# Optimization experiments

Hardware: AMD Instinct MI355X
Metric: run time of the kernel (lower is better)

## Reference

```python
import jax, jax.numpy as jnp
import numpy as np

D_MODEL = 512
NUM_HEADS = 8
D_FF = 2048
HEAD_DIM = D_MODEL // NUM_HEADS
EPS = 1e-8


def rmsnorm(x, scale):
    rms = jax.lax.rsqrt(jnp.mean(x * x, axis=-1, keepdims=True) + EPS)
    return scale * x * rms


def alibi_bias(seq_len, num_heads):
    # faithful to: 1.0 / (arange(1,H+1) * 2**arange(0,8)[:,None]).flatten()[:H]
    a = jnp.arange(1, num_heads + 1, dtype=jnp.float32)          # (H,)
    b = 2.0 ** jnp.arange(0, 8, dtype=jnp.float32)[:, None]       # (8,1)
    slopes = (1.0 / (a * b).reshape(-1))[:num_heads]               # (H,)
    pos = jnp.arange(seq_len)
    dist = jnp.abs(pos[:, None] - pos[None, :]).astype(jnp.float32)  # (S,S)
    return -slopes[:, None, None] * dist[None]                     # (H,S,S)


def setup_inputs() -> dict:
    key = jax.random.key(0)
    ks = jax.random.split(key, 12)
    s = 0.02
    return {
        "x": jax.random.normal(ks[0], (2, 2048, D_MODEL), dtype=jnp.float32),
        "norm1_scale": jnp.ones((D_MODEL,), jnp.float32),
        "norm2_scale": jnp.ones((D_MODEL,), jnp.float32),
        "in_proj_w": jax.random.normal(ks[1], (3 * D_MODEL, D_MODEL), jnp.float32) * s,
        "in_proj_b": jnp.zeros((3 * D_MODEL,), jnp.float32),
        "out_proj_w": jax.random.normal(ks[2], (D_MODEL, D_MODEL), jnp.float32) * s,
        "out_proj_b": jnp.zeros((D_MODEL,), jnp.float32),
        "w1": jax.random.normal(ks[3], (D_FF, D_MODEL), jnp.float32) * s,
        "b1": jnp.zeros((D_FF,), jnp.float32),
        "w2": jax.random.normal(ks[4], (D_MODEL, D_FF), jnp.float32) * s,
        "b2": jnp.zeros((D_MODEL,), jnp.float32),
    }


def reference(x, norm1_scale, norm2_scale, in_proj_w, in_proj_b,
              out_proj_w, out_proj_b, w1, b1, w2, b2):
    B, S, D = x.shape
    xn = rmsnorm(x, norm1_scale)
    qkv = xn @ in_proj_w.T + in_proj_b                      # (B,S,3D)
    q, k, v = jnp.split(qkv, 3, axis=-1)
    q = q.reshape(B, S, NUM_HEADS, HEAD_DIM)
    k = k.reshape(B, S, NUM_HEADS, HEAD_DIM)
    v = v.reshape(B, S, NUM_HEADS, HEAD_DIM)
    scale = 1.0 / jnp.sqrt(jnp.float32(HEAD_DIM))
    scores = jnp.einsum('bqhd,bkhd->bhqk', q, k) * scale    # (B,H,S,S)
    scores = scores + alibi_bias(S, NUM_HEADS)[None]
    attn = jax.nn.softmax(scores, axis=-1)
    ctx = jnp.einsum('bhqk,bkhd->bqhd', attn, v).reshape(B, S, D)
    attn_out = ctx @ out_proj_w.T + out_proj_b
    x = x + attn_out                                        # dropout is identity (eval)
    xn2 = rmsnorm(x, norm2_scale)
    h = jax.nn.gelu(xn2 @ w1.T + b1, approximate=False)
    mlp_out = h @ w2.T + b2
    return x + mlp_out
```

## Files before the change

### kernel.cpp

```cpp
#include <hip/hip_runtime.h>
#include <math.h>


typedef __bf16 bf16x8 __attribute__((ext_vector_type(8)));
typedef float  f32x4  __attribute__((ext_vector_type(4)));

#define TOKENS 4096
#define DMODEL 512
#define SEQ    2048
#define QSCALE 0.1803368801f

__device__ __forceinline__ void gl_lds16(const __bf16* g, __bf16* l) {
    __builtin_amdgcn_global_load_lds(
        (const __attribute__((address_space(1))) void*)g,
        (__attribute__((address_space(3))) void*)l, 16, 0, 0);
}

union PkU { unsigned u; __bf16 h[2]; };

__global__ void pre_kernel(const float* __restrict__ x, const float* __restrict__ n1s,
                           __bf16* __restrict__ xn1,
                           const float* __restrict__ w0, const float* __restrict__ w1,
                           const float* __restrict__ w2, const float* __restrict__ w3,
                           __bf16* __restrict__ d0, __bf16* __restrict__ d1,
                           __bf16* __restrict__ d2, __bf16* __restrict__ d3) {
    if (blockIdx.x < 1024) {
        int wave = threadIdx.x >> 6, lane = threadIdx.x & 63;
        int tok = blockIdx.x * 4 + wave;
        const float* row = x + (size_t)tok * DMODEL;
        float4 v0 = *(const float4*)&row[lane * 4];
        float4 v1 = *(const float4*)&row[256 + lane * 4];
        float ss = v0.x*v0.x + v0.y*v0.y + v0.z*v0.z + v0.w*v0.w
                 + v1.x*v1.x + v1.y*v1.y + v1.z*v1.z + v1.w*v1.w;
        #pragma unroll
        for (int off = 1; off < 64; off <<= 1) ss += __shfl_xor(ss, off);
        float r = rsqrtf(ss * (1.0f / DMODEL) + 1e-8f);
        __bf16* o = xn1 + (size_t)tok * DMODEL;
        o[lane*4 + 0] = (__bf16)(v0.x * r * n1s[lane*4 + 0]);
        o[lane*4 + 1] = (__bf16)(v0.y * r * n1s[lane*4 + 1]);
        o[lane*4 + 2] = (__bf16)(v0.z * r * n1s[lane*4 + 2]);
        o[lane*4 + 3] = (__bf16)(v0.w * r * n1s[lane*4 + 3]);
        o[256 + lane*4 + 0] = (__bf16)(v1.x * r * n1s[256 + lane*4 + 0]);
        o[256 + lane*4 + 1] = (__bf16)(v1.y * r * n1s[256 + lane*4 + 1]);
        o[256 + lane*4 + 2] = (__bf16)(v1.z * r * n1s[256 + lane*4 + 2]);
        o[256 + lane*4 + 3] = (__bf16)(v1.w * r * n1s[256 + lane*4 + 3]);
    } else {
        const int N0 = 1536 * 512, N1 = 512 * 512, N2 = 2048 * 512, N3 = 512 * 2048;
        int i4 = ((blockIdx.x - 1024) * 256 + threadIdx.x) * 4;
        const float* s; __bf16* d;
        if (i4 < N0)              { s = w0 + i4;  d = d0 + i4; }
        else if ((i4 -= N0) < N1) { s = w1 + i4;  d = d1 + i4; }
        else if ((i4 -= N1) < N2) { s = w2 + i4;  d = d2 + i4; }
        else if ((i4 -= N2) < N3) { s = w3 + i4;  d = d3 + i4; }
        else return;
        float4 v = *(const float4*)s;
        d[0] = (__bf16)v.x; d[1] = (__bf16)v.y; d[2] = (__bf16)v.z; d[3] = (__bf16)v.w;
    }
}

__global__ void rmsnorm2_kernel(const __bf16* __restrict__ x1b, const float* __restrict__ scale,
                                const float* __restrict__ b2,
                                __bf16* __restrict__ xn2, float* __restrict__ outInit) {
    int wave = threadIdx.x >> 6, lane = threadIdx.x & 63;
    int tok = blockIdx.x * 4 + wave;
    bf16x8 v = *(const bf16x8*)&x1b[(size_t)tok * DMODEL + lane * 8];
    float f[8], ss = 0.0f;
    #pragma unroll
    for (int j = 0; j < 8; j++) { f[j] = (float)v[j]; ss += f[j] * f[j]; }
    #pragma unroll
    for (int off = 1; off < 64; off <<= 1) ss += __shfl_xor(ss, off);
    float r = rsqrtf(ss * (1.0f / DMODEL) + 1e-8f);
    bf16x8 o;
    float4 s0 = *(const float4*)&scale[lane * 8];
    float4 s1 = *(const float4*)&scale[lane * 8 + 4];
    o[0] = (__bf16)(f[0]*r*s0.x); o[1] = (__bf16)(f[1]*r*s0.y);
    o[2] = (__bf16)(f[2]*r*s0.z); o[3] = (__bf16)(f[3]*r*s0.w);
    o[4] = (__bf16)(f[4]*r*s1.x); o[5] = (__bf16)(f[5]*r*s1.y);
    o[6] = (__bf16)(f[6]*r*s1.z); o[7] = (__bf16)(f[7]*r*s1.w);
    *(bf16x8*)&xn2[(size_t)tok * DMODEL + lane * 8] = o;
    float4 b0 = *(const float4*)&b2[lane * 8];
    float4 b1 = *(const float4*)&b2[lane * 8 + 4];
    float4 w0 = make_float4(f[0] + b0.x, f[1] + b0.y, f[2] + b0.z, f[3] + b0.w);
    float4 w1 = make_float4(f[4] + b1.x, f[5] + b1.y, f[6] + b1.z, f[7] + b1.w);
    *(float4*)&outInit[(size_t)tok * DMODEL + lane * 8] = w0;
    *(float4*)&outInit[(size_t)tok * DMODEL + lane * 8 + 4] = w1;
}

template <int EPI, int TM, int KS = 1>
__global__ __launch_bounds__(256) void gemm_bt(
    const __bf16* __restrict__ A, const __bf16* __restrict__ W,
    const float* __restrict__ bias, const float* __restrict__ res,
    float* __restrict__ Cf, __bf16* __restrict__ Cb,
    __bf16* __restrict__ qb, __bf16* __restrict__ kb, __bf16* __restrict__ vtb,
    int M, int N, int K)
{
    constexpr int RI = TM / 32;
    __shared__ alignas(16) __bf16 As[2][TM * 32];
    __shared__ alignas(16) __bf16 Bs[2][128 * 32];
    const int tid = threadIdx.x;
    const int bm = blockIdx.x * TM;
    const int bn = blockIdx.y * 128;
    const int wave = tid >> 6, lane = tid & 63;
    const int wm = (wave & 1) * (TM / 2), wn = (wave >> 1) * 64;
    const int lrow = lane & 15;
    const int kq = (lane >> 4) * 8;

    f32x4 acc[RI][4] = {};

    const int Kc = K / KS;
    const int kbeg = (KS > 1) ? blockIdx.z * Kc : 0;

    for (int k0 = kbeg; k0 < kbeg + Kc; k0 += 64) {
        __syncthreads();
        #pragma unroll
        for (int i = 0; i < TM / 32; i++) {
            int tt = i * 256 + tid;
            int kh = tt / (TM * 4), rem = tt % (TM * 4);
            int mrow = rem >> 2, c8 = rem & 3;
            gl_lds16(&A[(size_t)(bm + mrow) * K + k0 + kh * 32 + c8 * 8],
                     (__bf16*)As + tt * 8);
        }
        #pragma unroll
        for (int i = 0; i < 4; i++) {
            int tt = i * 256 + tid;
            int kh = tt >> 9, rem = tt & 511;
            int nrow = rem >> 2, c8 = rem & 3;
            gl_lds16(&W[(size_t)(bn + nrow) * K + k0 + kh * 32 + c8 * 8],
                     (__bf16*)Bs + tt * 8);
        }
        __syncthreads();
        #pragma unroll
        for (int kh = 0; kh < 2; kh++) {
            bf16x8 af[RI], bfv[4];
            #pragma unroll
            for (int i = 0; i < RI; i++) af[i] = *(bf16x8*)&As[kh][(wm + i*16 + lrow)*32 + kq];
            #pragma unroll
            for (int j = 0; j < 4; j++) bfv[j] = *(bf16x8*)&Bs[kh][(wn + j*16 + lrow)*32 + kq];
            #pragma unroll
            for (int i = 0; i < RI; i++)
                #pragma unroll
                for (int j = 0; j < 4; j++)
                    acc[i][j] = __builtin_amdgcn_mfma_f32_16x16x32_bf16(af[i], bfv[j], acc[i][j], 0, 0, 0);
        }
    }

    const int crow0 = (lane >> 4) * 4;
    const int ccol = lane & 15;
    const int quad = lane >> 4;

    if (EPI == 4) {
        #pragma unroll
        for (int j = 0; j < 4; j++) {
            const int col = bn + wn + j * 16 + ccol;
            const float bv = bias[col];
            if (col < 512) {
                const int h = col >> 6, d = col & 63;
                #pragma unroll
                for (int i = 0; i < RI; i++) {
                    const int row0 = bm + wm + i * 16 + crow0;
                    const int b = row0 >> 11, s0 = row0 & 2047;
                    #pragma unroll
                    for (int r = 0; r < 4; r++)
                        qb[(((size_t)b*8 + h)*2048 + s0 + r)*64 + d] =
                            (__bf16)((acc[i][j][r] + bv) * QSCALE);
                }
            } else if (col < 1024) {
                const int h = (col - 512) >> 6, d = col & 63;
                #pragma unroll
                for (int i = 0; i < RI; i++) {
                    const int row0 = bm + wm + i * 16 + crow0;
                    const int b = row0 >> 11, s0 = row0 & 2047;
                    #pragma unroll
                    for (int r = 0; r < 4; r++)
                        kb[(((size_t)b*8 + h)*2048 + s0 + r)*64 + d] = (__bf16)(acc[i][j][r] + bv);
                }
            } else {
                const int h = (col - 1024) >> 6, d = col & 63;
                const int tok0 = bm + wm;
                const int b = tok0 >> 11, sbase = tok0 & 2047;
                unsigned* vrow = (unsigned*)vtb + (((size_t)b*8 + h)*64 + d) * 1024 + (sbase >> 1);
                #pragma unroll
                for (int ip = 0; ip < RI / 2; ip++) {
                    #pragma unroll
                    for (int r = 0; r < 4; r++) {
                        PkU pk;
                        pk.h[0] = (__bf16)(acc[2*ip][j][r] + bv);
                        pk.h[1] = (__bf16)(acc[2*ip+1][j][r] + bv);
                        vrow[ip * 16 + quad * 4 + r] = pk.u;
                    }
                }
            }
        }
    } else {
        #pragma unroll
        for (int i = 0; i < RI; i++) {
            const int row0 = bm + wm + i * 16 + crow0;
            #pragma unroll
            for (int j = 0; j < 4; j++) {
                const int col = bn + wn + j * 16 + ccol;
                if (EPI == 7) {
                    const float bv = bias[col];
                    #pragma unroll
                    for (int r = 0; r < 4; r++) {
                        const size_t idx = (size_t)(row0 + r) * N + col;
                        Cb[idx] = (__bf16)(res[idx] + acc[i][j][r] + bv);
                    }
                } else if (EPI == 2) {
                    const float bv = bias[col];
                    #pragma unroll
                    for (int r = 0; r < 4; r++) {
                        float v = acc[i][j][r] + bv;
                        float u = v * (0.7978845608f + 0.0356774081f * v * v);
                        float t = exp2f(u * 2.8853900818f);
                        Cb[(size_t)(row0 + r) * N + col] = (__bf16)(v - v / (t + 1.0f));
                    }
                } else {
                    #pragma unroll
                    for (int r = 0; r < 4; r++)
                        unsafeAtomicAdd(&Cf[(size_t)(row0 + r) * N + col], acc[i][j][r]);
                }
            }
        }
    }
}

__global__ __launch_bounds__(256) void attn_kernel(
    const __bf16* __restrict__ qb, const __bf16* __restrict__ kb,
    const __bf16* __restrict__ vtb, __bf16* __restrict__ ctx)
{
    const int id = blockIdx.x;
    const int qt = id >> 4;
    const int bh = (id & 15) ^ (7 * (id >> 8));
    const int h = bh & 7, b = bh >> 3;
    const int tid = threadIdx.x, wave = tid >> 6, lane = tid & 63;
    const int lrow = lane & 15, quad = lane >> 4;

    __shared__ alignas(16) __bf16 Ks[2][2][64 * 32];
    __shared__ alignas(16) __bf16 Vt[2][2][64 * 32];
    __shared__ alignas(16) unsigned Pt4[4][2][16][20];

    const float slope2 = -1.44269504f / (float)(h + 1);
    const int q0 = qt * 64;
    const int D = 16 * (h + 1) + 16;
    const int kt_lo = max(0, q0 - D) >> 6;
    const int kt_hi = min(SEQ - 1, q0 + 63 + D) >> 6;

    bf16x8 qf[2];
    #pragma unroll
    for (int dh = 0; dh < 2; dh++)
        qf[dh] = *(const bf16x8*)&qb[((size_t)bh*2048 + q0 + wave*16 + lrow)*64 + dh*32 + quad*8];

    bf16x8 ones;
    #pragma unroll
    for (int j = 0; j < 8; j++) ones[j] = (__bf16)1.0f;

    f32x4 O[4] = {};
    f32x4 lacc = {};

    auto stage = [&](int kt, int buf) {
        const int kbase = kt * 64;
        #pragma unroll
        for (int i = 0; i < 2; i++) {
            int tt = i * 256 + tid;
            int dh = tt >> 8, key = (tt & 255) >> 2, c8 = (tt & 3) * 8;
            gl_lds16(&kb[((size_t)bh*2048 + kbase + key)*64 + dh*32 + c8],
                     (__bf16*)Ks[buf] + tt * 8);
        }
        #pragma unroll
        for (int i = 0; i < 2; i++) {
            int tt = i * 256 + tid;
            int kh = tt >> 8, d = (tt & 255) >> 2, ck = (tt & 3) * 8;
            gl_lds16(&vtb[((size_t)bh*64 + d)*2048 + kbase + kh*32 + ck],
                     (__bf16*)Vt[buf] + tt * 8);
        }
    };

    stage(kt_lo, 0);

    for (int kt = kt_lo, buf = 0; kt <= kt_hi; kt++, buf ^= 1) {
        __syncthreads();
        if (kt < kt_hi) stage(kt + 1, buf ^ 1);

        bf16x8 kf[4][2];
        #pragma unroll
        for (int j = 0; j < 4; j++)
            #pragma unroll
            for (int dh = 0; dh < 2; dh++)
                kf[j][dh] = *(bf16x8*)&Ks[buf][dh][(j*16 + lrow)*32 + quad*8];

        f32x4 Sc[4] = {};
        #pragma unroll
        for (int dh = 0; dh < 2; dh++)
            #pragma unroll
            for (int j = 0; j < 4; j++)
                Sc[j] = __builtin_amdgcn_mfma_f32_16x16x32_bf16(qf[dh], kf[j][dh], Sc[j], 0, 0, 0);

        const float dbase = (float)(q0 + wave*16 + quad*4 - kt*64 - lrow);
        #pragma unroll
        for (int r = 0; r < 4; r++) {
            const float d0 = dbase + (float)r;
            #pragma unroll
            for (int jp = 0; jp < 2; jp++) {
                float v0 = fmaf(slope2, fabsf(d0 - (float)(jp*32)),      Sc[2*jp  ][r]);
                float v1 = fmaf(slope2, fabsf(d0 - (float)(jp*32 + 16)), Sc[2*jp+1][r]);
                PkU pk;
                pk.h[0] = (__bf16)exp2f(v0);
                pk.h[1] = (__bf16)exp2f(v1);
                Pt4[wave][jp][quad*4 + r][lrow] = pk.u;
            }
        }

        bf16x8 pf[2];
        #pragma unroll
        for (int kh = 0; kh < 2; kh++)
            pf[kh] = *(bf16x8*)&Pt4[wave][kh][lrow][quad*4];

        #pragma unroll
        for (int kh = 0; kh < 2; kh++)
            lacc = __builtin_amdgcn_mfma_f32_16x16x32_bf16(pf[kh], ones, lacc, 0, 0, 0);

        #pragma unroll
        for (int dt = 0; dt < 4; dt++) {
            #pragma unroll
            for (int kh = 0; kh < 2; kh++) {
                bf16x8 vf = *(bf16x8*)&Vt[buf][kh][(dt*16 + lrow)*32 + quad*8];
                O[dt] = __builtin_amdgcn_mfma_f32_16x16x32_bf16(pf[kh], vf, O[dt], 0, 0, 0);
            }
        }
    }

    #pragma unroll
    for (int dt = 0; dt < 4; dt++) {
        #pragma unroll
        for (int r = 0; r < 4; r++) {
            const int q = q0 + wave*16 + quad*4 + r;
            ctx[((size_t)(b * 2048 + q)) * DMODEL + h * 64 + dt*16 + lrow] =
                (__bf16)(O[dt][r] / lacc[r]);
        }
    }
}

extern "C" void kernel_launch(void* const* d_in, const int* in_sizes, int n_in,
                              void* d_out, int out_size, void* d_ws, size_t ws_size,
                              hipStream_t stream) {
    const float* x    = (const float*)d_in[0];
    const float* n1s  = (const float*)d_in[1];
    const float* n2s  = (const float*)d_in[2];
    const float* wqkv = (const float*)d_in[3];
    const float* bqkv = (const float*)d_in[4];
    const float* wout = (const float*)d_in[5];
    const float* bout = (const float*)d_in[6];
    const float* w1   = (const float*)d_in[7];
    const float* b1   = (const float*)d_in[8];
    const float* w2   = (const float*)d_in[9];
    const float* b2   = (const float*)d_in[10];
    float* out = (float*)d_out;

    char* ws = (char*)d_ws;
    __bf16* xn1     = (__bf16*)ws; ws += (size_t)TOKENS * DMODEL * 2;
    __bf16* qbuf    = (__bf16*)ws; ws += (size_t)TOKENS * DMODEL * 2;
    __bf16* kbuf    = (__bf16*)ws; ws += (size_t)TOKENS * DMODEL * 2;
    __bf16* vtbuf   = (__bf16*)ws; ws += (size_t)TOKENS * DMODEL * 2;
    __bf16* wqkv_b  = (__bf16*)ws; ws += (size_t)1536 * DMODEL * 2;
    __bf16* wout_b  = (__bf16*)ws; ws += (size_t)DMODEL * DMODEL * 2;
    __bf16* w1_b    = (__bf16*)ws; ws += (size_t)2048 * DMODEL * 2;
    __bf16* w2_b    = (__bf16*)ws; ws += (size_t)DMODEL * 2048 * 2;
    __bf16* ctx     = (__bf16*)ws; ws += (size_t)TOKENS * DMODEL * 2;
    __bf16* x1b     = (__bf16*)ws; ws += (size_t)TOKENS * DMODEL * 2;
    __bf16* xn2     = (__bf16*)ws; ws += (size_t)TOKENS * DMODEL * 2;
    __bf16* hbuf    = (__bf16*)ws; ws += (size_t)TOKENS * 2048 * 2;

    pre_kernel<<<dim3(4096), 256, 0, stream>>>(x, n1s, xn1,
        wqkv, wout, w1, w2, wqkv_b, wout_b, w1_b, w2_b);

    gemm_bt<4, 64><<<dim3(TOKENS / 64, 1536 / 128), 256, 0, stream>>>(
        xn1, wqkv_b, bqkv, nullptr, nullptr, nullptr, qbuf, kbuf, vtbuf,
        TOKENS, 1536, DMODEL);

    attn_kernel<<<dim3(512), 256, 0, stream>>>(qbuf, kbuf, vtbuf, ctx);

    gemm_bt<7, 32><<<dim3(TOKENS / 32, DMODEL / 128), 256, 0, stream>>>(
        ctx, wout_b, bout, x, nullptr, x1b, nullptr, nullptr, nullptr,
        TOKENS, DMODEL, DMODEL);

    rmsnorm2_kernel<<<dim3(TOKENS / 4), 256, 0, stream>>>(x1b, n2s, b2, xn2, out);

    gemm_bt<2, 64><<<dim3(TOKENS / 64, 2048 / 128), 256, 0, stream>>>(
        xn2, w1_b, b1, nullptr, nullptr, hbuf, nullptr, nullptr, nullptr,
        TOKENS, 2048, DMODEL);

    gemm_bt<5, 32, 4><<<dim3(TOKENS / 32, DMODEL / 128, 4), 256, 0, stream>>>(
        hbuf, w2_b, nullptr, nullptr, out, nullptr, nullptr, nullptr, nullptr,
        TOKENS, DMODEL, 2048);
}
```

Measured before the change: 179.3 us.

## Fold second RMSNorm into out-proj and FFN1 GEMM epilogues, drop rmsnorm2 kernel

Removes the standalone rmsnorm2 kernel. The out-projection epilogue now writes the residual in bf16 and the fp32 output init (residual plus b2), and atomically accumulates per-row sum of squares. The norm2 scale is folded into the bf16 W1 copy, and the FFN1 epilogue applies the per-row rsqrt to the accumulator before bias and GELU. This saves one launch and one activation round trip, at the cost of extra atomics, a zeroing block, and x1b being quantized before the norm. Separately, the FFN2 split-K factor drops from 4 to 2.

```diff
diff --git a/kernel.cpp b/kernel.cpp
--- a/kernel.cpp
+++ b/kernel.cpp
@@ -19,11 +19,12 @@
 union PkU { unsigned u; __bf16 h[2]; };
 
 __global__ void pre_kernel(const float* __restrict__ x, const float* __restrict__ n1s,
-                           __bf16* __restrict__ xn1,
-                           const float* __restrict__ w0, const float* __restrict__ w1,
-                           const float* __restrict__ w2, const float* __restrict__ w3,
-                           __bf16* __restrict__ d0, __bf16* __restrict__ d1,
-                           __bf16* __restrict__ d2, __bf16* __restrict__ d3) {
+                           const float* __restrict__ n2s, __bf16* __restrict__ xn1,
+                           const float* __restrict__ wa, const float* __restrict__ wb,
+                           const float* __restrict__ wc, const float* __restrict__ wd,
+                           __bf16* __restrict__ da, __bf16* __restrict__ db,
+                           __bf16* __restrict__ dc, __bf16* __restrict__ dd,
+                           float* __restrict__ rssum) {
     if (blockIdx.x < 1024) {
         int wave = threadIdx.x >> 6, lane = threadIdx.x & 63;
         int tok = blockIdx.x * 4 + wave;
@@ -44,46 +45,36 @@
         o[256 + lane*4 + 1] = (__bf16)(v1.y * r * n1s[256 + lane*4 + 1]);
         o[256 + lane*4 + 2] = (__bf16)(v1.z * r * n1s[256 + lane*4 + 2]);
         o[256 + lane*4 + 3] = (__bf16)(v1.w * r * n1s[256 + lane*4 + 3]);
-    } else {
+    } else if (blockIdx.x < 4096) {
         const int N0 = 1536 * 512, N1 = 512 * 512, N2 = 2048 * 512, N3 = 512 * 2048;
         int i4 = ((blockIdx.x - 1024) * 256 + threadIdx.x) * 4;
-        const float* s; __bf16* d;
-        if (i4 < N0)              { s = w0 + i4;  d = d0 + i4; }
-        else if ((i4 -= N0) < N1) { s = w1 + i4;  d = d1 + i4; }
-        else if ((i4 -= N1) < N2) { s = w2 + i4;  d = d2 + i4; }
-        else if ((i4 -= N2) < N3) { s = w3 + i4;  d = d3 + i4; }
-        else return;
-        float4 v = *(const float4*)s;
-        d[0] = (__bf16)v.x; d[1] = (__bf16)v.y; d[2] = (__bf16)v.z; d[3] = (__bf16)v.w;
+        if (i4 < N0) {
+            float4 v = *(const float4*)&wa[i4];
+            __bf16* d = da + i4;
+            d[0] = (__bf16)v.x; d[1] = (__bf16)v.y; d[2] = (__bf16)v.z; d[3] = (__bf16)v.w;
+        } else if ((i4 -= N0) < N1) {
+            float4 v = *(const float4*)&wb[i4];
+            __bf16* d = db + i4;
+            d[0] = (__bf16)v.x; d[1] = (__bf16)v.y; d[2] = (__bf16)v.z; d[3] = (__bf16)v.w;
+        } else if ((i4 -= N1) < N2) {
+            float4 v = *(const float4*)&wc[i4];
+            float4 sc = *(const float4*)&n2s[i4 & 511];
+            __bf16* d = dc + i4;
+            d[0] = (__bf16)(v.x * sc.x); d[1] = (__bf16)(v.y * sc.y);
+            d[2] = (__bf16)(v.z * sc.z); d[3] = (__bf16)(v.w * sc.w);
+        } else if ((i4 -= N2) < N3) {
+            float4 v = *(const float4*)&wd[i4];
+            __bf16* d = dd + i4;
+            d[0] = (__bf16)v.x; d[1] = (__bf16)v.y; d[2] = (__bf16)v.z; d[3] = (__bf16)v.w;
+        }
+    } else {
+        float4 z = make_float4(0.f, 0.f, 0.f, 0.f);
+        int i = threadIdx.x * 16;
+        *(float4*)&rssum[i + 0]  = z;
+        *(float4*)&rssum[i + 4]  = z;
+        *(float4*)&rssum[i + 8]  = z;
+        *(float4*)&rssum[i + 12] = z;
     }
-}
-
-__global__ void rmsnorm2_kernel(const __bf16* __restrict__ x1b, const float* __restrict__ scale,
-                                const float* __restrict__ b2,
-                                __bf16* __restrict__ xn2, float* __restrict__ outInit) {
-    int wave = threadIdx.x >> 6, lane = threadIdx.x & 63;
-    int tok = blockIdx.x * 4 + wave;
-    bf16x8 v = *(const bf16x8*)&x1b[(size_t)tok * DMODEL + lane * 8];
-    float f[8], ss = 0.0f;
-    #pragma unroll
-    for (int j = 0; j < 8; j++) { f[j] = (float)v[j]; ss += f[j] * f[j]; }
-    #pragma unroll
-    for (int off = 1; off < 64; off <<= 1) ss += __shfl_xor(ss, off);
-    float r = rsqrtf(ss * (1.0f / DMODEL) + 1e-8f);
-    bf16x8 o;
-    float4 s0 = *(const float4*)&scale[lane * 8];
-    float4 s1 = *(const float4*)&scale[lane * 8 + 4];
-    o[0] = (__bf16)(f[0]*r*s0.x); o[1] = (__bf16)(f[1]*r*s0.y);
-    o[2] = (__bf16)(f[2]*r*s0.z); o[3] = (__bf16)(f[3]*r*s0.w);
-    o[4] = (__bf16)(f[4]*r*s1.x); o[5] = (__bf16)(f[5]*r*s1.y);
-    o[6] = (__bf16)(f[6]*r*s1.z); o[7] = (__bf16)(f[7]*r*s1.w);
-    *(bf16x8*)&xn2[(size_t)tok * DMODEL + lane * 8] = o;
-    float4 b0 = *(const float4*)&b2[lane * 8];
-    float4 b1 = *(const float4*)&b2[lane * 8 + 4];
-    float4 w0 = make_float4(f[0] + b0.x, f[1] + b0.y, f[2] + b0.z, f[3] + b0.w);
-    float4 w1 = make_float4(f[4] + b1.x, f[5] + b1.y, f[6] + b1.z, f[7] + b1.w);
-    *(float4*)&outInit[(size_t)tok * DMODEL + lane * 8] = w0;
-    *(float4*)&outInit[(size_t)tok * DMODEL + lane * 8 + 4] = w1;
 }
 
 template <int EPI, int TM, int KS = 1>
@@ -92,6 +83,7 @@
     const float* __restrict__ bias, const float* __restrict__ res,
     float* __restrict__ Cf, __bf16* __restrict__ Cb,
     __bf16* __restrict__ qb, __bf16* __restrict__ kb, __bf16* __restrict__ vtb,
+    const float* __restrict__ b2x, float* __restrict__ rssum,
     int M, int N, int K)
 {
     constexpr int RI = TM / 32;
@@ -195,26 +187,53 @@
         #pragma unroll
         for (int i = 0; i < RI; i++) {
             const int row0 = bm + wm + i * 16 + crow0;
-            #pragma unroll
-            for (int j = 0; j < 4; j++) {
-                const int col = bn + wn + j * 16 + ccol;
-                if (EPI == 7) {
+            if (EPI == 9) {
+                float rms[4];
+                #pragma unroll
+                for (int r = 0; r < 4; r++)
+                    rms[r] = rsqrtf(rssum[row0 + r] * (1.0f / 512.0f) + 1e-8f);
+                #pragma unroll
+                for (int j = 0; j < 4; j++) {
+                    const int col = bn + wn + j * 16 + ccol;
                     const float bv = bias[col];
                     #pragma unroll
                     for (int r = 0; r < 4; r++) {
-                        const size_t idx = (size_t)(row0 + r) * N + col;
-                        Cb[idx] = (__bf16)(res[idx] + acc[i][j][r] + bv);
-                    }
-                } else if (EPI == 2) {
-                    const float bv = bias[col];
-                    #pragma unroll
-                    for (int r = 0; r < 4; r++) {
-                        float v = acc[i][j][r] + bv;
+                        float v = acc[i][j][r] * rms[r] + bv;
                         float u = v * (0.7978845608f + 0.0356774081f * v * v);
                         float t = exp2f(u * 2.8853900818f);
                         Cb[(size_t)(row0 + r) * N + col] = (__bf16)(v - v / (t + 1.0f));
                     }
-                } else {
+                }
+            } else if (EPI == 8) {
+                float ssq[4] = {};
+                #pragma unroll
+                for (int j = 0; j < 4; j++) {
+                    const int col = bn + wn + j * 16 + ccol;
+                    const float bv = bias[col], b2v = b2x[col];
+                    #pragma unroll
+                    for (int r = 0; r < 4; r++) {
+                        const size_t idx = (size_t)(row0 + r) * N + col;
+                        float v = res[idx] + acc[i][j][r] + bv;
+                        Cb[idx] = (__bf16)v;
+                        Cf[idx] = v + b2v;
+                        ssq[r] += v * v;
+                    }
+                }
+                #pragma unroll
+                for (int r = 0; r < 4; r++) {
+                    #pragma unroll
+                    for (int off = 1; off < 16; off <<= 1)
+                        ssq[r] += __shfl_xor(ssq[r], off);
+                }
+                if (ccol == 0) {
+                    #pragma unroll
+                    for (int r = 0; r < 4; r++)
+                        unsafeAtomicAdd(&rssum[row0 + r], ssq[r]);
+                }
+            } else {
+                #pragma unroll
+                for (int j = 0; j < 4; j++) {
+                    const int col = bn + wn + j * 16 + ccol;
                     #pragma unroll
                     for (int r = 0; r < 4; r++)
                         unsafeAtomicAdd(&Cf[(size_t)(row0 + r) * N + col], acc[i][j][r]);
@@ -363,33 +382,31 @@
     __bf16* vtbuf   = (__bf16*)ws; ws += (size_t)TOKENS * DMODEL * 2;
     __bf16* wqkv_b  = (__bf16*)ws; ws += (size_t)1536 * DMODEL * 2;
     __bf16* wout_b  = (__bf16*)ws; ws += (size_t)DMODEL * DMODEL * 2;
-    __bf16* w1_b    = (__bf16*)ws; ws += (size_t)2048 * DMODEL * 2;
+    __bf16* w1n_b   = (__bf16*)ws; ws += (size_t)2048 * DMODEL * 2;
     __bf16* w2_b    = (__bf16*)ws; ws += (size_t)DMODEL * 2048 * 2;
     __bf16* ctx     = (__bf16*)ws; ws += (size_t)TOKENS * DMODEL * 2;
     __bf16* x1b     = (__bf16*)ws; ws += (size_t)TOKENS * DMODEL * 2;
-    __bf16* xn2     = (__bf16*)ws; ws += (size_t)TOKENS * DMODEL * 2;
     __bf16* hbuf    = (__bf16*)ws; ws += (size_t)TOKENS * 2048 * 2;
-
-    pre_kernel<<<dim3(4096), 256, 0, stream>>>(x, n1s, xn1,
-        wqkv, wout, w1, w2, wqkv_b, wout_b, w1_b, w2_b);
+    float*  rssum   = (float*)ws;  ws += (size_t)TOKENS * 4;
+
+    pre_kernel<<<dim3(4097), 256, 0, stream>>>(x, n1s, n2s, xn1,
+        wqkv, wout, w1, w2, wqkv_b, wout_b, w1n_b, w2_b, rssum);
 
     gemm_bt<4, 64><<<dim3(TOKENS / 64, 1536 / 128), 256, 0, stream>>>(
         xn1, wqkv_b, bqkv, nullptr, nullptr, nullptr, qbuf, kbuf, vtbuf,
-        TOKENS, 1536, DMODEL);
+        nullptr, nullptr, TOKENS, 1536, DMODEL);
 
     attn_kernel<<<dim3(512), 256, 0, stream>>>(qbuf, kbuf, vtbuf, ctx);
 
-    gemm_bt<7, 32><<<dim3(TOKENS / 32, DMODEL / 128), 256, 0, stream>>>(
-        ctx, wout_b, bout, x, nullptr, x1b, nullptr, nullptr, nullptr,
-        TOKENS, DMODEL, DMODEL);
-
-    rmsnorm2_kernel<<<dim3(TOKENS / 4), 256, 0, stream>>>(x1b, n2s, b2, xn2, out);
-
-    gemm_bt<2, 64><<<dim3(TOKENS / 64, 2048 / 128), 256, 0, stream>>>(
-        xn2, w1_b, b1, nullptr, nullptr, hbuf, nullptr, nullptr, nullptr,
-        TOKENS, 2048, DMODEL);
-
-    gemm_bt<5, 32, 4><<<dim3(TOKENS / 32, DMODEL / 128, 4), 256, 0, stream>>>(
+    gemm_bt<8, 32><<<dim3(TOKENS / 32, DMODEL / 128), 256, 0, stream>>>(
+        ctx, wout_b, bout, x, out, x1b, nullptr, nullptr, nullptr,
+        b2, rssum, TOKENS, DMODEL, DMODEL);
+
+    gemm_bt<9, 64><<<dim3(TOKENS / 64, 2048 / 128), 256, 0, stream>>>(
+        x1b, w1n_b, b1, nullptr, nullptr, hbuf, nullptr, nullptr, nullptr,
+        nullptr, rssum, TOKENS, 2048, DMODEL);
+
+    gemm_bt<5, 32, 2><<<dim3(TOKENS / 32, DMODEL / 128, 2), 256, 0, stream>>>(
         hbuf, w2_b, nullptr, nullptr, out, nullptr, nullptr, nullptr, nullptr,
-        TOKENS, DMODEL, 2048);
+        nullptr, nullptr, TOKENS, DMODEL, 2048);
 }
```

Measured after the change: 167.7 us (median of 2 runs). 1.07x faster.
